# Performance work log

Measured on AMD Instinct MI355X. Metric: run time of the kernel, lower is better.

The kernel has to match this reference:

```python
import jax, jax.numpy as jnp
import numpy as np

B, S, HID = 2, 2048, 4096
H, KVH, D = 32, 8, 128
MAXPOS = 4096


def _rotate_half(x):
    x1, x2 = jnp.split(x, 2, axis=-1)
    return jnp.concatenate([-x2, x1], axis=-1)


def setup_inputs() -> dict:
    key = jax.random.key(0)
    k0, k1, k2, k3, k4 = jax.random.split(key, 5)
    s = 0.02
    hidden_states = jax.random.normal(k0, (B, S, HID), jnp.float32)
    Wq = jax.random.normal(k1, (HID, H * D), jnp.float32) * s
    Wk = jax.random.normal(k2, (HID, KVH * D), jnp.float32) * s
    Wv = jax.random.normal(k3, (HID, KVH * D), jnp.float32) * s
    Wo = jax.random.normal(k4, (H * D, HID), jnp.float32) * s
    past_key_value = jnp.zeros((B, 2, KVH, MAXPOS, D), jnp.float32)
    # RoPE tables (fp32, as asserted in the torch module)
    inv_freq = 1.0 / (10000.0 ** (np.arange(0, D, 2, dtype=np.float64) / D))
    freqs = np.outer(np.arange(S, dtype=np.float64), inv_freq)  # [S, D/2]
    emb = np.concatenate([freqs, freqs], axis=-1)                # [S, D]
    cos = jnp.asarray(np.cos(emb), jnp.float32)
    sin = jnp.asarray(np.sin(emb), jnp.float32)
    return {"hidden_states": hidden_states, "past_key_value": past_key_value,
            "cos": cos, "sin": sin, "Wq": Wq, "Wk": Wk, "Wv": Wv, "Wo": Wo}


def reference(hidden_states, past_key_value, cos, sin, Wq, Wk, Wv, Wo):
    b, s, _ = hidden_states.shape
    # QKV projections (no bias, as in Llama-style attention)
    q = (hidden_states @ Wq).reshape(b, s, H, D)
    k = (hidden_states @ Wk).reshape(b, s, KVH, D)
    v = (hidden_states @ Wv).reshape(b, s, KVH, D)
    # Fused RoPE (qk_norm is identity for standard models)
    c = cos[None, :, None, :]
    sn = sin[None, :, None, :]
    q = q * c + _rotate_half(q) * sn
    k = k * c + _rotate_half(k) * sn
    # KV-cache update (prefill: context_lengths=0, kvcache_start_index=0)
    k_bhsd = k.transpose(0, 2, 1, 3)  # [b, kvh, s, d]
    v_bhsd = v.transpose(0, 2, 1, 3)
    present = past_key_value.at[:, 0, :, :s, :].set(k_bhsd)
    present = present.at[:, 1, :, :s, :].set(v_bhsd)
    # GQA: repeat kv heads to match query heads
    rep = H // KVH
    kr = jnp.repeat(k, rep, axis=2)  # [b, s, H, d]
    vr = jnp.repeat(v, rep, axis=2)
    scores = jnp.einsum("bqhd,bkhd->bhqk", q, kr) / np.float32(np.sqrt(D))
    causal = jnp.tril(jnp.ones((s, s), bool))  # [q, k]
    scores = jnp.where(causal[None, None], scores, jnp.finfo(scores.dtype).min)
    w = jax.nn.softmax(scores.astype(jnp.float32), axis=-1).astype(q.dtype)
    attn = jnp.einsum("bhqk,bkhd->bqhd", w, vr).reshape(b, s, H * D)
    out = attn @ Wo
    return out, present
```

## Files before the change

kernel.cpp:

```cpp
#include <hip/hip_runtime.h>
#include <hip/hip_bf16.h>

typedef unsigned short u16;
typedef __bf16 bf16x8 __attribute__((ext_vector_type(8)));
typedef float  f32x4  __attribute__((ext_vector_type(4)));

__device__ __forceinline__ u16 f2bf(float f) {
    return __builtin_bit_cast(u16, (__bf16)f);
}
__device__ __forceinline__ f32x4 mfma16(bf16x8 a, bf16x8 b, f32x4 c) {
    return __builtin_amdgcn_mfma_f32_16x16x32_bf16(a, b, c, 0, 0, 0);
}
__device__ __forceinline__ void gl_lds16(const void* g, void* l) {
    __builtin_amdgcn_global_load_lds((const __attribute__((address_space(1))) void*)g,
                                     (__attribute__((address_space(3))) void*)l, 16, 0, 0);
}

__global__ void k_cast_bf16(const float* __restrict__ src, u16* __restrict__ dst) {
    long i = ((long)blockIdx.x * blockDim.x + threadIdx.x) * 4;
    float4 v = *(const float4*)(src + i);
    ushort4 o;
    o.x = f2bf(v.x); o.y = f2bf(v.y); o.z = f2bf(v.z); o.w = f2bf(v.w);
    *(ushort4*)(dst + i) = o;
}

__global__ void k_transpose_cvt(const float* __restrict__ src, u16* __restrict__ dst,
                                int K, int N) {
    __shared__ float t[32][33];
    int n0 = blockIdx.x * 32, k0 = blockIdx.y * 32;
    int tx = threadIdx.x, ty = threadIdx.y;
    #pragma unroll
    for (int i = 0; i < 32; i += 8)
        t[ty + i][tx] = src[(long)(k0 + ty + i) * N + n0 + tx];
    __syncthreads();
    #pragma unroll
    for (int i = 0; i < 32; i += 8)
        dst[(long)(n0 + ty + i) * K + k0 + tx] = f2bf(t[tx][ty + i]);
}

__global__ void k_copy_half(const float4* __restrict__ src, float4* __restrict__ dst) {
    long i = (long)blockIdx.x * 256 + threadIdx.x;
    long g = i >> 16;
    long inner = i & 65535;
    long off = g * 131072 + 65536 + inner;
    dst[off] = src[off];
}

template<int BNF>
__global__ void __launch_bounds__(512, 2)
k_gemm8(const u16* __restrict__ A, const u16* __restrict__ Bt,
        float* __restrict__ C, int M, int N, int K, int gx)
{
    extern __shared__ u16 lds[];
    const int nwg = gridDim.x;
    const int bid = blockIdx.x;
    const int swzb = (bid & 7) * (nwg >> 3) + (bid >> 3);
    const long m0 = (long)(swzb / gx) * 256;
    const long n0 = (long)(swzb % gx) * (64 * BNF);

    const int t = threadIdx.x;
    const int l = t & 63;
    const int w = t >> 6;
    const int wm = w >> 2, wn = w & 3;

    const int srow = t >> 3;
    const int scol = ((t & 7) ^ (srow & 7)) << 3;
    const u16* ap = A  + (m0 + srow) * (long)K + scol;
    const u16* bp = Bt + (n0 + srow) * (long)K + scol;
    const int sL = t * 8;

    const int swz0 = (((l >> 4) ^ (l & 7)) << 3);
    const int swz1 = ((((l >> 4) | 4) ^ (l & 7)) << 3);
    const int arow = wm * 128 + (l & 15);
    const int aoff0 = arow * 64 + swz0, aoff1 = arow * 64 + swz1;
    const int brow = wn * (16 * BNF) + (l & 15);
    const int boff0 = brow * 64 + swz0, boff1 = brow * 64 + swz1;

    f32x4 acc[8][BNF];
    #pragma unroll
    for (int i = 0; i < 8; ++i)
        #pragma unroll
        for (int j = 0; j < BNF; ++j) acc[i][j] = (f32x4){0.f, 0.f, 0.f, 0.f};

    const int nt = K >> 6;
    #pragma unroll
    for (int k = 0; k < 4; ++k)
        gl_lds16(ap + (long)k * 64 * K, &lds[sL + 4096 * k]);
    #pragma unroll
    for (int k = 0; k < BNF; ++k)
        gl_lds16(bp + (long)k * 64 * K, &lds[32768 + sL + 4096 * k]);

    for (int kt = 0; kt < nt; ++kt) {
        const int d = kt & 1;
        const int dA = d * 16384, dB = 32768 + d * 4096 * BNF;
        if (kt + 1 < nt) {
            const int e = d ^ 1;
            const u16* a1 = ap + (kt + 1) * 64;
            const u16* b1 = bp + (kt + 1) * 64;
            #pragma unroll
            for (int k = 0; k < 4; ++k)
                gl_lds16(a1 + (long)k * 64 * K, &lds[e * 16384 + sL + 4096 * k]);
            #pragma unroll
            for (int k = 0; k < BNF; ++k)
                gl_lds16(b1 + (long)k * 64 * K, &lds[32768 + e * 4096 * BNF + sL + 4096 * k]);
            if constexpr (BNF == 3) asm volatile("s_waitcnt vmcnt(7)" ::: "memory");
            else                    asm volatile("s_waitcnt vmcnt(8)" ::: "memory");
        } else {
            asm volatile("s_waitcnt vmcnt(0)" ::: "memory");
        }
        __builtin_amdgcn_sched_barrier(0);
        __builtin_amdgcn_s_barrier();
        __builtin_amdgcn_sched_barrier(0);

        bf16x8 bfr[BNF][2];
        #pragma unroll
        for (int nf = 0; nf < BNF; ++nf) {
            bfr[nf][0] = *(const bf16x8*)&lds[dB + boff0 + nf * 1024];
            bfr[nf][1] = *(const bf16x8*)&lds[dB + boff1 + nf * 1024];
        }
        {
            bf16x8 af[2][2];
            #pragma unroll
            for (int mm = 0; mm < 2; ++mm) {
                af[mm][0] = *(const bf16x8*)&lds[dA + aoff0 + mm * 1024];
                af[mm][1] = *(const bf16x8*)&lds[dA + aoff1 + mm * 1024];
            }
            asm volatile("s_waitcnt lgkmcnt(0)" ::: "memory");
            __builtin_amdgcn_sched_barrier(0);
            __builtin_amdgcn_s_setprio(1);
            #pragma unroll
            for (int mm = 0; mm < 2; ++mm)
                #pragma unroll
                for (int nf = 0; nf < BNF; ++nf) {
                    acc[mm][nf] = mfma16(af[mm][0], bfr[nf][0], acc[mm][nf]);
                    acc[mm][nf] = mfma16(af[mm][1], bfr[nf][1], acc[mm][nf]);
                }
            __builtin_amdgcn_s_setprio(0);
            __builtin_amdgcn_sched_barrier(0);
        }
        #pragma unroll
        for (int q = 1; q < 4; ++q) {
            bf16x8 af[2][2];
            #pragma unroll
            for (int mm = 0; mm < 2; ++mm) {
                af[mm][0] = *(const bf16x8*)&lds[dA + aoff0 + (q * 2 + mm) * 1024];
                af[mm][1] = *(const bf16x8*)&lds[dA + aoff1 + (q * 2 + mm) * 1024];
            }
            __builtin_amdgcn_sched_barrier(0);
            __builtin_amdgcn_s_barrier();
            asm volatile("s_waitcnt lgkmcnt(0)" ::: "memory");
            __builtin_amdgcn_sched_barrier(0);
            __builtin_amdgcn_s_setprio(1);
            #pragma unroll
            for (int mm = 0; mm < 2; ++mm)
                #pragma unroll
                for (int nf = 0; nf < BNF; ++nf) {
                    acc[q * 2 + mm][nf] = mfma16(af[mm][0], bfr[nf][0], acc[q * 2 + mm][nf]);
                    acc[q * 2 + mm][nf] = mfma16(af[mm][1], bfr[nf][1], acc[q * 2 + mm][nf]);
                }
            __builtin_amdgcn_s_setprio(0);
            __builtin_amdgcn_sched_barrier(0);
        }
        __builtin_amdgcn_s_barrier();
        __builtin_amdgcn_sched_barrier(0);
    }

    #pragma unroll
    for (int mf = 0; mf < 8; ++mf)
        #pragma unroll
        for (int nf = 0; nf < BNF; ++nf) {
            long row = m0 + wm * 128 + mf * 16 + ((l >> 4) << 2);
            float* cp = C + row * N + n0 + wn * (16 * BNF) + nf * 16 + (l & 15);
            #pragma unroll
            for (int r = 0; r < 4; ++r) cp[(long)r * N] = acc[mf][nf][r];
        }
}

__global__ void k_rope_scatter(const float* __restrict__ qkv, const float* __restrict__ cosb,
                               const float* __restrict__ sinb, u16* __restrict__ Qb,
                               u16* __restrict__ Kb, u16* __restrict__ Vt,
                               float* __restrict__ present)
{
    long idx = (long)blockIdx.x * 256 + threadIdx.x;
    int pg   = (int)(idx & 15);
    int rem  = (int)(idx >> 4);
    int slot = rem % 48;
    int tok  = rem / 48;
    int b = tok >> 11, s = tok & 2047;
    int pair = pg * 4;

    const float* base = qkv + (long)tok * 6144 + slot * 128 + pair;
    float4 x1 = *(const float4*)(base);
    float4 x2 = *(const float4*)(base + 64);

    if (slot < 40) {
        float4 c  = *(const float4*)(cosb + s * 128 + pair);
        float4 sn = *(const float4*)(sinb + s * 128 + pair);
        float4 y1, y2;
        y1.x = x1.x * c.x - x2.x * sn.x;  y2.x = x2.x * c.x + x1.x * sn.x;
        y1.y = x1.y * c.y - x2.y * sn.y;  y2.y = x2.y * c.y + x1.y * sn.y;
        y1.z = x1.z * c.z - x2.z * sn.z;  y2.z = x2.z * c.z + x1.z * sn.z;
        y1.w = x1.w * c.w - x2.w * sn.w;  y2.w = x2.w * c.w + x1.w * sn.w;
        if (slot < 32) {
            const float sc = 0.0883883476483184f;
            long qoff = (((long)b * 32 + slot) * 2048 + s) * 128 + pair;
            ushort4 o1, o2;
            o1.x = f2bf(y1.x * sc); o1.y = f2bf(y1.y * sc);
            o1.z = f2bf(y1.z * sc); o1.w = f2bf(y1.w * sc);
            o2.x = f2bf(y2.x * sc); o2.y = f2bf(y2.y * sc);
            o2.z = f2bf(y2.z * sc); o2.w = f2bf(y2.w * sc);
            *(ushort4*)(Qb + qoff)      = o1;
            *(ushort4*)(Qb + qoff + 64) = o2;
        } else {
            int kvh = slot - 32;
            long koff = (((long)b * 8 + kvh) * 2048 + s) * 128 + pair;
            ushort4 o1, o2;
            o1.x = f2bf(y1.x); o1.y = f2bf(y1.y); o1.z = f2bf(y1.z); o1.w = f2bf(y1.w);
            o2.x = f2bf(y2.x); o2.y = f2bf(y2.y); o2.z = f2bf(y2.z); o2.w = f2bf(y2.w);
            *(ushort4*)(Kb + koff)      = o1;
            *(ushort4*)(Kb + koff + 64) = o2;
            long poff = ((((long)b * 2 + 0) * 8 + kvh) * 4096 + s) * 128 + pair;
            *(float4*)(present + poff)      = y1;
            *(float4*)(present + poff + 64) = y2;
        }
    } else {
        int kvh = slot - 40;
        long poff = ((((long)b * 2 + 1) * 8 + kvh) * 4096 + s) * 128 + pair;
        *(float4*)(present + poff)      = x1;
        *(float4*)(present + poff + 64) = x2;
        long voff = (((long)b * 8 + kvh) * 128 + pair) * 2048 + s;
        Vt[voff]                  = f2bf(x1.x);
        Vt[voff + 1 * 2048]       = f2bf(x1.y);
        Vt[voff + 2 * 2048]       = f2bf(x1.z);
        Vt[voff + 3 * 2048]       = f2bf(x1.w);
        Vt[voff + 64 * 2048]      = f2bf(x2.x);
        Vt[voff + 65 * 2048]      = f2bf(x2.y);
        Vt[voff + 66 * 2048]      = f2bf(x2.z);
        Vt[voff + 67 * 2048]      = f2bf(x2.w);
    }
}

__global__ void __launch_bounds__(256, 2)
k_attn(const u16* __restrict__ Qb, const u16* __restrict__ Kb,
       const u16* __restrict__ Vt, u16* __restrict__ attnB)
{
    __shared__ __align__(16) u16 Ks[2][64 * 128];
    __shared__ __align__(16) u16 Vs[2][128 * 64];
    __shared__ __align__(16) u16 Ps[4][32 * 64];
    const int l = threadIdx.x & 63;
    const int w = threadIdx.x >> 6;
    const int h = blockIdx.y, b = blockIdx.z;
    const int p = blockIdx.x;
    const int kvh = h >> 2;
    u16* Psw = &Ps[w][0];

    const long kbase = ((long)b * 8 + kvh) * (2048L * 128);
    const long vbase = ((long)b * 8 + kvh) * (128L * 2048);
    f32x4 zero = {0.f, 0.f, 0.f, 0.f};

    const int ck  = w * 4;
    const int krow0 = ck * 4 + (l >> 4);
    const int vrow0 = ck * 8 + (l >> 3);
    const int vlg0  = ((l & 7) ^ (vrow0 & 7)) << 3;

    for (int half = 0; half < 2; ++half) {
        const int qt = half ? (15 - p) : p;
        const int q0 = qt * 128;

        const long qbase = (((long)b * 32 + h) * 2048 + q0 + w * 32) * 128;
        bf16x8 qf[2][4];
        #pragma unroll
        for (int mi = 0; mi < 2; ++mi)
            #pragma unroll
            for (int kk = 0; kk < 4; ++kk)
                qf[mi][kk] = *(const bf16x8*)(Qb + qbase + (long)(mi * 16 + (l & 15)) * 128
                                              + kk * 32 + ((l >> 4) << 3));

        f32x4 o[2][8];
        float mst[2][4], lst[2][4];
        #pragma unroll
        for (int mi = 0; mi < 2; ++mi) {
            #pragma unroll
            for (int j = 0; j < 8; ++j) o[mi][j] = zero;
            #pragma unroll
            for (int r = 0; r < 4; ++r) { mst[mi][r] = -3.0e38f; lst[mi][r] = 0.f; }
        }

        const int nkt = (q0 >> 6) + 2;

        #pragma unroll
        for (int i = 0; i < 4; ++i) {
            int c = ck + i;
            int krow = krow0 + i * 4;
            int klg = ((l & 15) ^ (krow & 15)) << 3;
            gl_lds16(Kb + kbase + (long)krow * 128 + klg, &Ks[0][c * 512]);
            gl_lds16(Vt + vbase + (long)(vrow0 + i * 8) * 2048 + vlg0, &Vs[0][c * 512]);
        }

        for (int kt = 0; kt < nkt; ++kt) {
            const int d = kt & 1;
            if (kt + 1 < nkt) {
                const int e = d ^ 1;
                const int k1 = (kt + 1) * 64;
                #pragma unroll
                for (int i = 0; i < 4; ++i) {
                    int c = ck + i;
                    int krow = krow0 + i * 4;
                    int klg = ((l & 15) ^ (krow & 15)) << 3;
                    gl_lds16(Kb + kbase + (long)(k1 + krow) * 128 + klg, &Ks[e][c * 512]);
                    gl_lds16(Vt + vbase + (long)(vrow0 + i * 8) * 2048 + k1 + vlg0,
                             &Vs[e][c * 512]);
                }
                asm volatile("s_waitcnt vmcnt(8)" ::: "memory");
            } else {
                asm volatile("s_waitcnt vmcnt(0)" ::: "memory");
            }
            __builtin_amdgcn_sched_barrier(0);
            __builtin_amdgcn_s_barrier();
            __builtin_amdgcn_sched_barrier(0);

            const int k0 = kt * 64;
            f32x4 s[2][4];
            #pragma unroll
            for (int mi = 0; mi < 2; ++mi)
                #pragma unroll
                for (int nf = 0; nf < 4; ++nf) s[mi][nf] = zero;
            #pragma unroll
            for (int kk = 0; kk < 4; ++kk) {
                bf16x8 kf[4];
                #pragma unroll
                for (int nf = 0; nf < 4; ++nf) {
                    int row = nf * 16 + (l & 15);
                    int ph = (kk * 4 + (l >> 4)) ^ (row & 15);
                    kf[nf] = *(const bf16x8*)&Ks[d][row * 128 + ph * 8];
                }
                #pragma unroll
                for (int mi = 0; mi < 2; ++mi)
                    #pragma unroll
                    for (int nf = 0; nf < 4; ++nf)
                        s[mi][nf] = mfma16(qf[mi][kk], kf[nf], s[mi][nf]);
            }
            #pragma unroll
            for (int mi = 0; mi < 2; ++mi)
                #pragma unroll
                for (int nf = 0; nf < 4; ++nf)
                    #pragma unroll
                    for (int r = 0; r < 4; ++r) {
                        int rowg = q0 + w * 32 + mi * 16 + ((l >> 4) << 2) + r;
                        int colg = k0 + nf * 16 + (l & 15);
                        if (colg > rowg) s[mi][nf][r] = -1.0e30f;
                    }
            #pragma unroll
            for (int mi = 0; mi < 2; ++mi)
                #pragma unroll
                for (int r = 0; r < 4; ++r) {
                    float t = fmaxf(fmaxf(s[mi][0][r], s[mi][1][r]),
                                    fmaxf(s[mi][2][r], s[mi][3][r]));
                    t = fmaxf(t, __shfl_xor(t, 1));
                    t = fmaxf(t, __shfl_xor(t, 2));
                    t = fmaxf(t, __shfl_xor(t, 4));
                    t = fmaxf(t, __shfl_xor(t, 8));
                    float nm = fmaxf(mst[mi][r], t);
                    float sc = __expf(mst[mi][r] - nm);
                    mst[mi][r] = nm;
                    lst[mi][r] *= sc;
                    #pragma unroll
                    for (int nf2 = 0; nf2 < 8; ++nf2) o[mi][nf2][r] *= sc;
                }
            #pragma unroll
            for (int mi = 0; mi < 2; ++mi)
                #pragma unroll
                for (int nf = 0; nf < 4; ++nf)
                    #pragma unroll
                    for (int r = 0; r < 4; ++r) {
                        float pv = __expf(s[mi][nf][r] - mst[mi][r]);
                        lst[mi][r] += pv;
                        int row = mi * 16 + ((l >> 4) << 2) + r;
                        int col = nf * 16 + (l & 15);
                        Psw[row * 64 + (((col >> 3) ^ (row & 7)) << 3) + (col & 7)] = f2bf(pv);
                    }
            #pragma unroll
            for (int kk2 = 0; kk2 < 2; ++kk2) {
                bf16x8 pa[2];
                #pragma unroll
                for (int mi = 0; mi < 2; ++mi) {
                    int row = mi * 16 + (l & 15);
                    int ph = (kk2 * 4 + (l >> 4)) ^ (row & 7);
                    pa[mi] = *(const bf16x8*)&Psw[row * 64 + ph * 8];
                }
                #pragma unroll
                for (int nf2 = 0; nf2 < 8; ++nf2) {
                    int vrow = nf2 * 16 + (l & 15);
                    int ph = (kk2 * 4 + (l >> 4)) ^ (vrow & 7);
                    bf16x8 vf = *(const bf16x8*)&Vs[d][vrow * 64 + ph * 8];
                    #pragma unroll
                    for (int mi = 0; mi < 2; ++mi)
                        o[mi][nf2] = mfma16(pa[mi], vf, o[mi][nf2]);
                }
            }
            __builtin_amdgcn_sched_barrier(0);
            __builtin_amdgcn_s_barrier();
            __builtin_amdgcn_sched_barrier(0);
        }

        #pragma unroll
        for (int mi = 0; mi < 2; ++mi)
            #pragma unroll
            for (int r = 0; r < 4; ++r) {
                float t = lst[mi][r];
                t += __shfl_xor(t, 1);
                t += __shfl_xor(t, 2);
                t += __shfl_xor(t, 4);
                t += __shfl_xor(t, 8);
                lst[mi][r] = 1.0f / t;
            }
        #pragma unroll
        for (int mi = 0; mi < 2; ++mi)
            #pragma unroll
            for (int nf2 = 0; nf2 < 8; ++nf2)
                #pragma unroll
                for (int r = 0; r < 4; ++r) {
                    long row = (long)b * 2048 + q0 + w * 32 + mi * 16 + ((l >> 4) << 2) + r;
                    attnB[row * 4096 + h * 128 + nf2 * 16 + (l & 15)] =
                        f2bf(o[mi][nf2][r] * lst[mi][r]);
                }
    }
}

extern "C" void kernel_launch(void* const* d_in, const int* in_sizes, int n_in,
                              void* d_out, int out_size, void* d_ws, size_t ws_size,
                              hipStream_t stream)
{
    (void)in_sizes; (void)n_in; (void)out_size; (void)ws_size;
    const float* hidden = (const float*)d_in[0];
    const float* past   = (const float*)d_in[1];
    const float* cosb   = (const float*)d_in[2];
    const float* sinb   = (const float*)d_in[3];
    const float* Wq     = (const float*)d_in[4];
    const float* Wk     = (const float*)d_in[5];
    const float* Wv     = (const float*)d_in[6];
    const float* Wo     = (const float*)d_in[7];
    float* out     = (float*)d_out;
    float* present = out + 16777216L;

    char* ws = (char*)d_ws;
    u16*  hiddenB = (u16*)(ws);
    u16*  WqkvT   = (u16*)(ws + 33554432L);
    u16*  WoT     = (u16*)(ws + 83886080L);
    float* QKVf   = (float*)(ws + 117440512L);
    u16*  Kb      = (u16*)(ws + 218103808L);
    u16*  Vt      = (u16*)(ws + 226492416L);
    u16*  Qbuf    = hiddenB;
    u16*  attnB   = (u16*)QKVf;

    static bool attr_done = false;
    if (!attr_done) {
        hipFuncSetAttribute((const void*)k_gemm8<3>,
                            hipFuncAttributeMaxDynamicSharedMemorySize, 114688);
        hipFuncSetAttribute((const void*)k_gemm8<4>,
                            hipFuncAttributeMaxDynamicSharedMemorySize, 131072);
        attr_done = true;
    }

    k_cast_bf16<<<16384, 256, 0, stream>>>(hidden, hiddenB);
    dim3 tb(32, 8);
    k_transpose_cvt<<<dim3(128, 128), tb, 0, stream>>>(Wq, WqkvT, 4096, 4096);
    k_transpose_cvt<<<dim3(32, 128),  tb, 0, stream>>>(Wk, WqkvT + 4096L * 4096, 4096, 1024);
    k_transpose_cvt<<<dim3(32, 128),  tb, 0, stream>>>(Wv, WqkvT + 5120L * 4096, 4096, 1024);
    k_transpose_cvt<<<dim3(128, 128), tb, 0, stream>>>(Wo, WoT, 4096, 4096);
    k_copy_half<<<8192, 256, 0, stream>>>((const float4*)past, (float4*)present);
    k_gemm8<3><<<512, 512, 114688, stream>>>(hiddenB, WqkvT, QKVf, 4096, 6144, 4096, 32);
    k_rope_scatter<<<12288, 256, 0, stream>>>(QKVf, cosb, sinb, Qbuf, Kb, Vt, present);
    k_attn<<<dim3(8, 32, 2), 256, 0, stream>>>(Qbuf, Kb, Vt, attnB);
    k_gemm8<4><<<256, 512, 131072, stream>>>(attnB, WoT, out, 4096, 4096, 4096, 16);
}
```

Baseline: 628.1 us.

## Single-buffer K/V tiles and alias P scratch into K buffer to cut LDS

Replaces the double-buffered K/V shared-memory tiles with single buffers and stores the per-wave softmax P tile inside the K tile region once QK^T is done. This shrinks LDS per block, presumably to let more blocks reside per CU. In exchange the overlap between the next tile's global-to-LDS load and the current tile's compute is lost, and an extra barrier is added before P is written into the aliased buffer. The loads are issued right after a __syncthreads with no explicit vmcnt wait, so correctness depends on the barrier also waiting on the LDS-direct loads.

```diff
diff --git a/kernel.cpp b/kernel.cpp
--- a/kernel.cpp
+++ b/kernel.cpp
@@ -244,25 +244,19 @@
 k_attn(const u16* __restrict__ Qb, const u16* __restrict__ Kb,
        const u16* __restrict__ Vt, u16* __restrict__ attnB)
 {
-    __shared__ __align__(16) u16 Ks[2][64 * 128];
-    __shared__ __align__(16) u16 Vs[2][128 * 64];
-    __shared__ __align__(16) u16 Ps[4][32 * 64];
+    __shared__ __align__(16) u16 Ks[64 * 128];
+    __shared__ __align__(16) u16 Vs[128 * 64];
     const int l = threadIdx.x & 63;
     const int w = threadIdx.x >> 6;
     const int h = blockIdx.y, b = blockIdx.z;
     const int p = blockIdx.x;
     const int kvh = h >> 2;
-    u16* Psw = &Ps[w][0];
+    u16* Psw = &Ks[w * 2048];
 
     const long kbase = ((long)b * 8 + kvh) * (2048L * 128);
     const long vbase = ((long)b * 8 + kvh) * (128L * 2048);
     f32x4 zero = {0.f, 0.f, 0.f, 0.f};
 
-    const int ck  = w * 4;
-    const int krow0 = ck * 4 + (l >> 4);
-    const int vrow0 = ck * 8 + (l >> 3);
-    const int vlg0  = ((l & 7) ^ (vrow0 & 7)) << 3;
-
     for (int half = 0; half < 2; ++half) {
         const int qt = half ? (15 - p) : p;
         const int q0 = qt * 128;
@@ -287,39 +281,25 @@
         }
 
         const int nkt = (q0 >> 6) + 2;
-
-        #pragma unroll
-        for (int i = 0; i < 4; ++i) {
-            int c = ck + i;
-            int krow = krow0 + i * 4;
-            int klg = ((l & 15) ^ (krow & 15)) << 3;
-            gl_lds16(Kb + kbase + (long)krow * 128 + klg, &Ks[0][c * 512]);
-            gl_lds16(Vt + vbase + (long)(vrow0 + i * 8) * 2048 + vlg0, &Vs[0][c * 512]);
-        }
-
         for (int kt = 0; kt < nkt; ++kt) {
-            const int d = kt & 1;
-            if (kt + 1 < nkt) {
-                const int e = d ^ 1;
-                const int k1 = (kt + 1) * 64;
-                #pragma unroll
-                for (int i = 0; i < 4; ++i) {
-                    int c = ck + i;
-                    int krow = krow0 + i * 4;
-                    int klg = ((l & 15) ^ (krow & 15)) << 3;
-                    gl_lds16(Kb + kbase + (long)(k1 + krow) * 128 + klg, &Ks[e][c * 512]);
-                    gl_lds16(Vt + vbase + (long)(vrow0 + i * 8) * 2048 + k1 + vlg0,
-                             &Vs[e][c * 512]);
-                }
-                asm volatile("s_waitcnt vmcnt(8)" ::: "memory");
-            } else {
-                asm volatile("s_waitcnt vmcnt(0)" ::: "memory");
-            }
-            __builtin_amdgcn_sched_barrier(0);
-            __builtin_amdgcn_s_barrier();
-            __builtin_amdgcn_sched_barrier(0);
-
             const int k0 = kt * 64;
+            __syncthreads();
+            #pragma unroll
+            for (int i = 0; i < 4; ++i) {
+                int c = w * 4 + i;
+                int row = c * 4 + (l >> 4);
+                int lg = ((l & 15) ^ (row & 15)) << 3;
+                gl_lds16(Kb + kbase + (long)(k0 + row) * 128 + lg, &Ks[c * 512]);
+            }
+            #pragma unroll
+            for (int i = 0; i < 4; ++i) {
+                int c = w * 4 + i;
+                int row = c * 8 + (l >> 3);
+                int lg = ((l & 7) ^ (row & 7)) << 3;
+                gl_lds16(Vt + vbase + (long)row * 2048 + k0 + lg, &Vs[c * 512]);
+            }
+            __syncthreads();
+
             f32x4 s[2][4];
             #pragma unroll
             for (int mi = 0; mi < 2; ++mi)
@@ -332,7 +312,7 @@
                 for (int nf = 0; nf < 4; ++nf) {
                     int row = nf * 16 + (l & 15);
                     int ph = (kk * 4 + (l >> 4)) ^ (row & 15);
-                    kf[nf] = *(const bf16x8*)&Ks[d][row * 128 + ph * 8];
+                    kf[nf] = *(const bf16x8*)&Ks[row * 128 + ph * 8];
                 }
                 #pragma unroll
                 for (int mi = 0; mi < 2; ++mi)
@@ -367,6 +347,7 @@
                     #pragma unroll
                     for (int nf2 = 0; nf2 < 8; ++nf2) o[mi][nf2][r] *= sc;
                 }
+            __syncthreads();
             #pragma unroll
             for (int mi = 0; mi < 2; ++mi)
                 #pragma unroll
@@ -392,15 +373,12 @@
                 for (int nf2 = 0; nf2 < 8; ++nf2) {
                     int vrow = nf2 * 16 + (l & 15);
                     int ph = (kk2 * 4 + (l >> 4)) ^ (vrow & 7);
-                    bf16x8 vf = *(const bf16x8*)&Vs[d][vrow * 64 + ph * 8];
+                    bf16x8 vf = *(const bf16x8*)&Vs[vrow * 64 + ph * 8];
                     #pragma unroll
                     for (int mi = 0; mi < 2; ++mi)
                         o[mi][nf2] = mfma16(pa[mi], vf, o[mi][nf2]);
                 }
             }
-            __builtin_amdgcn_sched_barrier(0);
-            __builtin_amdgcn_s_barrier();
-            __builtin_amdgcn_sched_barrier(0);
         }
 
         #pragma unroll
```

Result: no change. 619.6 us (-1.4%).
